# Optimization experiments

Measured on AMD Instinct MI355X. Metric: run time of the kernel, lower is better.

## Reference

```python
import jax, jax.numpy as jnp
import numpy as np

N = 100000      # nodes in batch / feature table
S = 25          # sampled neighbors per node (nsamples)
F_IN = 128      # in_features
F_OUT = 128     # out_features


def setup_inputs() -> dict:
    key = jax.random.key(0)
    k1, k2, k3, k4 = jax.random.split(key, 4)
    x = jax.random.normal(k1, (N, F_IN), dtype=jnp.float32)
    neighbor_idx = jax.random.randint(k2, (N, S), 0, N, dtype=jnp.int64)
    stdv = 1.0 / np.sqrt(F_OUT)
    W = jax.random.uniform(k3, (F_IN, F_OUT), dtype=jnp.float32, minval=-stdv, maxval=stdv)
    b = jax.random.uniform(k4, (F_OUT,), dtype=jnp.float32, minval=-stdv, maxval=stdv)
    return {"x": x, "neighbor_idx": neighbor_idx, "W": W, "b": b}


def reference(x, neighbor_idx, W, b):
    # GraphSage-style mean aggregator: gather sampled neighbor features
    # [N, S, F_IN], average together with the self feature, then project.
    neigh = jnp.take(x, neighbor_idx, axis=0)          # [N, S, F_IN] (irregular gather)
    agg = (x + neigh.sum(axis=1)) / jnp.float32(S + 1)  # mean over {self} U neighbors
    return agg @ W + b                                  # [N, F_OUT]
```

## Files before the change

### kernel.cpp

```cpp
#include <hip/hip_runtime.h>

#define F 128
#define S 25
#define CH 4
#define CW 32

typedef __attribute__((ext_vector_type(8))) short bf16x8;
typedef __attribute__((ext_vector_type(4))) float f32x4;
typedef __attribute__((ext_vector_type(2))) float f32x2;

__device__ __forceinline__ ushort f2bf(float f) {
    uint u = __float_as_uint(f);
    return (ushort)((u + 0x7FFFu + ((u >> 16) & 1u)) >> 16);
}
__device__ __forceinline__ float bf_lo(uint v) { return __uint_as_float(v << 16); }
__device__ __forceinline__ float bf_hi(uint v) { return __uint_as_float(v & 0xFFFF0000u); }

__device__ __forceinline__ bool idx_is_i64(const int* __restrict__ p) {
    return (p[1] | p[3] | p[5] | p[7]) == 0;
}
__device__ __forceinline__ int load_idx(const int* __restrict__ p, size_t i, bool is64) {
    return is64 ? p[2 * i] : p[i];
}

__global__ __launch_bounds__(256) void compact_idx(
    const int* __restrict__ src, int* __restrict__ dst, int M)
{
    const bool is64 = idx_is_i64(src);
    int e = blockIdx.x * 256 + threadIdx.x;
    if (e < M) dst[e] = load_idx(src, (size_t)e, is64);
}

template <int CHUNKED>
__global__ __launch_bounds__(256) void gemm_xw_bf16(
    const float* __restrict__ x, const float* __restrict__ W,
    ushort* __restrict__ y, int N)
{
    __shared__ ushort WF[4][8][64][8];

    const int tid  = threadIdx.x;
    const int lane = tid & 63;
    const int wid  = tid >> 6;

    for (int e = tid; e < 4 * 8 * 64; e += 256) {
        const int l  = e & 63;
        const int nt = (e >> 6) & 7;
        const int kt = e >> 9;
        const int k0 = kt * 32 + (l >> 4) * 8;
        const int n  = nt * 16 + (l & 15);
        #pragma unroll
        for (int b = 0; b < 8; ++b)
            WF[kt][nt][l][b] = f2bf(W[(size_t)(k0 + b) * F + n]);
    }
    __syncthreads();

    const int n0 = blockIdx.x * 64 + wid * 16;
    const int arow = n0 + (lane & 15);
    const int arow_c = arow < N ? arow : N - 1;
    const float* xrow = x + (size_t)arow_c * F + (lane >> 4) * 8;

    f32x4 acc[8];
    #pragma unroll
    for (int nt = 0; nt < 8; ++nt) acc[nt] = (f32x4){0.f, 0.f, 0.f, 0.f};

    #pragma unroll
    for (int kt = 0; kt < 4; ++kt) {
        float4 a0 = *(const float4*)(xrow + kt * 32);
        float4 a1 = *(const float4*)(xrow + kt * 32 + 4);
        bf16x8 af;
        af[0] = (short)f2bf(a0.x); af[1] = (short)f2bf(a0.y);
        af[2] = (short)f2bf(a0.z); af[3] = (short)f2bf(a0.w);
        af[4] = (short)f2bf(a1.x); af[5] = (short)f2bf(a1.y);
        af[6] = (short)f2bf(a1.z); af[7] = (short)f2bf(a1.w);
        #pragma unroll
        for (int nt = 0; nt < 8; ++nt) {
            bf16x8 bf = *(const bf16x8*)&WF[kt][nt][lane][0];
            acc[nt] = __builtin_amdgcn_mfma_f32_16x16x32_bf16(af, bf, acc[nt], 0, 0, 0);
        }
    }

    const int drow0 = n0 + (lane >> 4) * 4;
    const int dcol  = lane & 15;
    #pragma unroll
    for (int nt = 0; nt < 8; ++nt) {
        #pragma unroll
        for (int r = 0; r < 4; ++r) {
            const int row = drow0 + r;
            if (row < N) {
                if (CHUNKED) {
                    y[((size_t)(nt >> 1) * N + row) * CW + (nt & 1) * 16 + dcol] = f2bf(acc[nt][r]);
                } else {
                    y[(size_t)row * F + nt * 16 + dcol] = f2bf(acc[nt][r]);
                }
            }
        }
    }
}

__global__ __launch_bounds__(256) void gather_chunked(
    const ushort* __restrict__ y, const int* __restrict__ idx32,
    const float* __restrict__ bias, float* __restrict__ out, int N)
{
    __shared__ int IDX[64 * S];

    const int tid   = threadIdx.x;
    const int chunk = blockIdx.x & (CH - 1);
    const int tile  = blockIdx.x >> 2;
    const int nbase = tile * 64;
    const long total = (long)N * S;

    for (int e = tid; e < 64 * S; e += 256) {
        long p = (long)nbase * S + e;
        IDX[e] = (p < total) ? __builtin_nontemporal_load(&idx32[p]) : 0;
    }
    __syncthreads();

    const int lane = tid & 63, wave = tid >> 6;
    const int g = lane >> 4, j = lane & 15;
    const float2 bb = ((const float2*)bias)[chunk * (CW / 2) + j];
    const float inv = 1.0f / (float)(S + 1);
    const char* ycb = (const char*)(y + (size_t)chunk * N * CW);

    #pragma unroll
    for (int oct = 0; oct < 4; ++oct) {
        const int nl = wave * 16 + oct * 4 + g;
        const int n  = nbase + nl;
        const int nc = n < N ? n : 0;

        uint v[26];
        v[25] = *(const uint*)(ycb + (((uint)nc) << 6) + (j << 2));
        #pragma unroll
        for (int s = 0; s < S; ++s) {
            int id = IDX[nl * S + s];
            v[s] = *(const uint*)(ycb + (((uint)id) << 6) + (j << 2));
        }

        float ax = 0.f, ay = 0.f;
        #pragma unroll
        for (int s = 0; s < 26; ++s) { ax += bf_lo(v[s]); ay += bf_hi(v[s]); }

        if (n < N) {
            f32x2 o;
            o.x = ax * inv + bb.x;
            o.y = ay * inv + bb.y;
            __builtin_nontemporal_store(o, (f32x2*)(out + (size_t)n * F + chunk * CW + 2 * j));
        }
    }
}

__global__ __launch_bounds__(256) void gather_agg_bf16(
    const ushort* __restrict__ y, const int* __restrict__ nbr,
    const float* __restrict__ bias, float* __restrict__ out, int N)
{
    const int lane = threadIdx.x & 63;
    const int wid  = threadIdx.x >> 6;
    const bool is64 = idx_is_i64(nbr);
    const float2 bb = ((const float2*)bias)[lane];
    const float inv = 1.0f / (float)(S + 1);
    const int nw = gridDim.x * 4;
    const uint* yw = (const uint*)y;

    for (int n = blockIdx.x * 4 + wid; n < N; n += nw) {
        const int nu = __builtin_amdgcn_readfirstlane(n);
        int ids[S];
        #pragma unroll
        for (int s = 0; s < S; ++s)
            ids[s] = load_idx(nbr, (size_t)nu * S + s, is64);
        uint vs[S];
        #pragma unroll
        for (int s = 0; s < S; ++s)
            vs[s] = yw[(size_t)ids[s] * 64 + lane];
        const uint v0 = yw[(size_t)nu * 64 + lane];
        float ax = bf_lo(v0), ay = bf_hi(v0);
        #pragma unroll
        for (int s = 0; s < S; ++s) { ax += bf_lo(vs[s]); ay += bf_hi(vs[s]); }
        float2 o;
        o.x = ax * inv + bb.x;
        o.y = ay * inv + bb.y;
        ((float2*)(out + (size_t)nu * F))[lane] = o;
    }
}

__global__ __launch_bounds__(256) void fused_fallback_kernel(
    const float* __restrict__ x, const int* __restrict__ nbr,
    const float* __restrict__ W, const float* __restrict__ bias,
    float* __restrict__ out, int N)
{
    __shared__ float aggs[4][F];
    const int lane = threadIdx.x & 63;
    const int wid  = threadIdx.x >> 6;
    const bool is64 = idx_is_i64(nbr);
    const float inv = 1.0f / (float)(S + 1);
    const int stride = gridDim.x * 4;

    for (int base = blockIdx.x * 4; base < N; base += stride) {
        int n = base + wid;
        bool act = n < N;
        float2 acc = make_float2(0.f, 0.f);
        if (act) {
            acc = ((const float2*)(x + (size_t)n * F))[lane];
            for (int s = 0; s < S; ++s) {
                int id = load_idx(nbr, (size_t)n * S + s, is64);
                float2 v = ((const float2*)(x + (size_t)id * F))[lane];
                acc.x += v.x; acc.y += v.y;
            }
        }
        aggs[wid][2 * lane]     = acc.x * inv;
        aggs[wid][2 * lane + 1] = acc.y * inv;
        __syncthreads();
        if (act) {
            float o0 = bias[lane], o1 = bias[lane + 64];
            for (int k = 0; k < F; ++k) {
                float a = aggs[wid][k];
                o0 += a * W[k * F + lane];
                o1 += a * W[k * F + lane + 64];
            }
            out[(size_t)n * F + lane]      = o0;
            out[(size_t)n * F + lane + 64] = o1;
        }
        __syncthreads();
    }
}

extern "C" void kernel_launch(void* const* d_in, const int* in_sizes, int n_in,
                              void* d_out, int out_size, void* d_ws, size_t ws_size,
                              hipStream_t stream) {
    const float* x    = (const float*)d_in[0];
    const int*   nbr  = (const int*)d_in[1];
    const float* W    = (const float*)d_in[2];
    const float* bias = (const float*)d_in[3];
    float* out = (float*)d_out;
    const int N = in_sizes[0] / F;
    const int M = N * S;

    const size_t y_bytes   = (size_t)N * F * sizeof(ushort);
    const size_t idx_bytes = (size_t)M * sizeof(int);

    if (ws_size >= y_bytes + idx_bytes) {
        ushort* y   = (ushort*)d_ws;
        int*  idx32 = (int*)((char*)d_ws + y_bytes);
        compact_idx<<<(M + 255) / 256, 256, 0, stream>>>(nbr, idx32, M);
        gemm_xw_bf16<1><<<(N + 63) / 64, 256, 0, stream>>>(x, W, y, N);
        const int tiles = (N + 63) / 64;
        gather_chunked<<<tiles * CH, 256, 0, stream>>>(y, idx32, bias, out, N);
    } else if (ws_size >= y_bytes) {
        ushort* y = (ushort*)d_ws;
        gemm_xw_bf16<0><<<(N + 63) / 64, 256, 0, stream>>>(x, W, y, N);
        gather_agg_bf16<<<2048, 256, 0, stream>>>(y, nbr, bias, out, N);
    } else {
        fused_fallback_kernel<<<2048, 256, 0, stream>>>(x, nbr, W, bias, out, N);
    }
}
```

Measured before the change: 116.0 us.

## Prepack bf16 W fragments once and widen gather loads to 16 bytes

Adds a tiny pack_W kernel that converts and lays out W into MFMA fragment order in workspace once, so each GEMM block just copies 32KB with vector loads instead of redoing strided float loads and bf16 conversion. The chunked gather is restructured so each lane loads 16-byte uint4 neighbor slices (4 lanes per row segment, 16 nodes per wave) instead of 4-byte words over 4 iterations, with loads batched in two groups. This cuts per-block W setup cost and raises the width of each gather load, at the price of an extra launch, more registers, and less latency hiding across iterations.

```diff
diff --git a/kernel.cpp b/kernel.cpp
--- a/kernel.cpp
+++ b/kernel.cpp
@@ -16,6 +16,13 @@
 __device__ __forceinline__ float bf_lo(uint v) { return __uint_as_float(v << 16); }
 __device__ __forceinline__ float bf_hi(uint v) { return __uint_as_float(v & 0xFFFF0000u); }
 
+__device__ __forceinline__ void acc8(float* a, const uint4& v) {
+    a[0] += bf_lo(v.x); a[1] += bf_hi(v.x);
+    a[2] += bf_lo(v.y); a[3] += bf_hi(v.y);
+    a[4] += bf_lo(v.z); a[5] += bf_hi(v.z);
+    a[6] += bf_lo(v.w); a[7] += bf_hi(v.w);
+}
+
 __device__ __forceinline__ bool idx_is_i64(const int* __restrict__ p) {
     return (p[1] | p[3] | p[5] | p[7]) == 0;
 }
@@ -31,9 +38,26 @@
     if (e < M) dst[e] = load_idx(src, (size_t)e, is64);
 }
 
+__global__ __launch_bounds__(256) void pack_W(
+    const float* __restrict__ W, ushort* __restrict__ WFg)
+{
+    const int id = blockIdx.x * 256 + threadIdx.x;
+    if (id >= 4 * 8 * 64) return;
+    const int l  = id & 63;
+    const int nt = (id >> 6) & 7;
+    const int kt = id >> 9;
+    const int k0 = kt * 32 + (l >> 4) * 8;
+    const int nn = nt * 16 + (l & 15);
+    bf16x8 fr;
+    #pragma unroll
+    for (int b = 0; b < 8; ++b)
+        fr[b] = (short)f2bf(W[(size_t)(k0 + b) * F + nn]);
+    *(bf16x8*)(WFg + (size_t)id * 8) = fr;
+}
+
 template <int CHUNKED>
 __global__ __launch_bounds__(256) void gemm_xw_bf16(
-    const float* __restrict__ x, const float* __restrict__ W,
+    const float* __restrict__ x, const ushort* __restrict__ WFg,
     ushort* __restrict__ y, int N)
 {
     __shared__ ushort WF[4][8][64][8];
@@ -42,15 +66,12 @@
     const int lane = tid & 63;
     const int wid  = tid >> 6;
 
-    for (int e = tid; e < 4 * 8 * 64; e += 256) {
-        const int l  = e & 63;
-        const int nt = (e >> 6) & 7;
-        const int kt = e >> 9;
-        const int k0 = kt * 32 + (l >> 4) * 8;
-        const int n  = nt * 16 + (l & 15);
-        #pragma unroll
-        for (int b = 0; b < 8; ++b)
-            WF[kt][nt][l][b] = f2bf(W[(size_t)(k0 + b) * F + n]);
+    {
+        const bf16x8* src = (const bf16x8*)WFg;
+        bf16x8* dst = (bf16x8*)&WF[0][0][0][0];
+        #pragma unroll
+        for (int i = 0; i < 8; ++i)
+            dst[tid + 256 * i] = src[tid + 256 * i];
     }
     __syncthreads();
 
@@ -116,35 +137,49 @@
     __syncthreads();
 
     const int lane = tid & 63, wave = tid >> 6;
-    const int g = lane >> 4, j = lane & 15;
-    const float2 bb = ((const float2*)bias)[chunk * (CW / 2) + j];
+    const int g = lane >> 2, j = lane & 3;
+    const int nl = wave * 16 + g;
+    const int n  = nbase + nl;
+    const int nc = n < N ? n : 0;
     const float inv = 1.0f / (float)(S + 1);
     const char* ycb = (const char*)(y + (size_t)chunk * N * CW);
-
-    #pragma unroll
-    for (int oct = 0; oct < 4; ++oct) {
-        const int nl = wave * 16 + oct * 4 + g;
-        const int n  = nbase + nl;
-        const int nc = n < N ? n : 0;
-
-        uint v[26];
-        v[25] = *(const uint*)(ycb + (((uint)nc) << 6) + (j << 2));
-        #pragma unroll
-        for (int s = 0; s < S; ++s) {
-            int id = IDX[nl * S + s];
-            v[s] = *(const uint*)(ycb + (((uint)id) << 6) + (j << 2));
-        }
-
-        float ax = 0.f, ay = 0.f;
-        #pragma unroll
-        for (int s = 0; s < 26; ++s) { ax += bf_lo(v[s]); ay += bf_hi(v[s]); }
-
-        if (n < N) {
-            f32x2 o;
-            o.x = ax * inv + bb.x;
-            o.y = ay * inv + bb.y;
-            __builtin_nontemporal_store(o, (f32x2*)(out + (size_t)n * F + chunk * CW + 2 * j));
-        }
+    const int joff = j << 4;
+
+    float acc[8];
+    {
+        uint4 v = *(const uint4*)(ycb + (((uint)nc) << 6) + joff);
+        acc[0] = bf_lo(v.x); acc[1] = bf_hi(v.x);
+        acc[2] = bf_lo(v.y); acc[3] = bf_hi(v.y);
+        acc[4] = bf_lo(v.z); acc[5] = bf_hi(v.z);
+        acc[6] = bf_lo(v.w); acc[7] = bf_hi(v.w);
+    }
+
+    uint4 v[13];
+    #pragma unroll
+    for (int s = 0; s < 13; ++s) {
+        const int id = IDX[nl * S + s];
+        v[s] = *(const uint4*)(ycb + (((uint)id) << 6) + joff);
+    }
+    #pragma unroll
+    for (int s = 0; s < 13; ++s) acc8(acc, v[s]);
+
+    #pragma unroll
+    for (int s = 0; s < 12; ++s) {
+        const int id = IDX[nl * S + 13 + s];
+        v[s] = *(const uint4*)(ycb + (((uint)id) << 6) + joff);
+    }
+    #pragma unroll
+    for (int s = 0; s < 12; ++s) acc8(acc, v[s]);
+
+    if (n < N) {
+        const float* bp = bias + chunk * CW + j * 8;
+        float* op = out + (size_t)n * F + chunk * CW + j * 8;
+        f32x4 o0 = {acc[0] * inv + bp[0], acc[1] * inv + bp[1],
+                    acc[2] * inv + bp[2], acc[3] * inv + bp[3]};
+        f32x4 o1 = {acc[4] * inv + bp[4], acc[5] * inv + bp[5],
+                    acc[6] * inv + bp[6], acc[7] * inv + bp[7]};
+        __builtin_nontemporal_store(o0, (f32x4*)op);
+        __builtin_nontemporal_store(o1, (f32x4*)(op + 4));
     }
 }
 
@@ -235,17 +270,22 @@
 
     const size_t y_bytes   = (size_t)N * F * sizeof(ushort);
     const size_t idx_bytes = (size_t)M * sizeof(int);
-
-    if (ws_size >= y_bytes + idx_bytes) {
-        ushort* y   = (ushort*)d_ws;
-        int*  idx32 = (int*)((char*)d_ws + y_bytes);
+    const size_t wf_bytes  = (size_t)4 * 8 * 64 * 8 * sizeof(ushort);
+
+    if (ws_size >= y_bytes + idx_bytes + wf_bytes) {
+        ushort* y    = (ushort*)d_ws;
+        int*   idx32 = (int*)((char*)d_ws + y_bytes);
+        ushort* WFg  = (ushort*)((char*)d_ws + y_bytes + idx_bytes);
         compact_idx<<<(M + 255) / 256, 256, 0, stream>>>(nbr, idx32, M);
-        gemm_xw_bf16<1><<<(N + 63) / 64, 256, 0, stream>>>(x, W, y, N);
+        pack_W<<<8, 256, 0, stream>>>(W, WFg);
+        gemm_xw_bf16<1><<<(N + 63) / 64, 256, 0, stream>>>(x, WFg, y, N);
         const int tiles = (N + 63) / 64;
         gather_chunked<<<tiles * CH, 256, 0, stream>>>(y, idx32, bias, out, N);
-    } else if (ws_size >= y_bytes) {
-        ushort* y = (ushort*)d_ws;
-        gemm_xw_bf16<0><<<(N + 63) / 64, 256, 0, stream>>>(x, W, y, N);
+    } else if (ws_size >= y_bytes + wf_bytes) {
+        ushort* y   = (ushort*)d_ws;
+        ushort* WFg = (ushort*)((char*)d_ws + y_bytes);
+        pack_W<<<8, 256, 0, stream>>>(W, WFg);
+        gemm_xw_bf16<0><<<(N + 63) / 64, 256, 0, stream>>>(x, WFg, y, N);
         gather_agg_bf16<<<2048, 256, 0, stream>>>(y, nbr, bias, out, N);
     } else {
         fused_fallback_kernel<<<2048, 256, 0, stream>>>(x, nbr, W, bias, out, N);
```

New measurement: 133.9 us. 15.4% more time.
